# Kernel optimization log

Hardware: AMD Instinct MI355X
Metric: run time of the kernel (lower is better)

## Reference

```python
import jax, jax.numpy as jnp
import numpy as np

B, S, D, H = 4, 2048, 1024, 16
HD = D // H  # head dim = 64

def setup_inputs() -> dict:
    key = jax.random.key(0)
    ks = jax.random.split(key, 11)
    s = 1.0 / np.sqrt(D)
    return {
        "q": jax.random.normal(ks[0], (B, S, D), jnp.float32),
        "k": jax.random.normal(ks[1], (B, S, D), jnp.float32),
        "v": jax.random.normal(ks[2], (B, S, D), jnp.float32),
        "Wq": jax.random.normal(ks[3], (D, D), jnp.float32) * s,
        "bq": jnp.zeros((D,), jnp.float32),
        "Wk": jax.random.normal(ks[4], (D, D), jnp.float32) * s,
        "bk": jnp.zeros((D,), jnp.float32),
        "Wv": jax.random.normal(ks[5], (D, D), jnp.float32) * s,
        "bv": jnp.zeros((D,), jnp.float32),
        "Wo": jax.random.normal(ks[6], (D, D), jnp.float32) * s,
        "bo": jnp.zeros((D,), jnp.float32),
    }

def reference(q, k, v, Wq, bq, Wk, bk, Wv, bv, Wo, bo):
    b, n, _ = q.shape
    # QKV projections, split heads -> [b, s, h, hd]
    qh = (q @ Wq + bq).reshape(b, n, H, HD)
    kh = (k @ Wk + bk).reshape(b, k.shape[1], H, HD)
    vh = (v @ Wv + bv).reshape(b, v.shape[1], H, HD)
    scale = 1.0 / np.sqrt(HD)
    scores = jnp.einsum('blhe,bshe->bhls', qh, kh)  # [b,h,l,s]
    attn = jax.nn.softmax(scale * scores, axis=-1)  # dropout is identity in eval
    out = jnp.einsum('bhls,bshd->blhd', attn, vh)   # [b,l,h,hd]
    out = out.reshape(b, n, H * HD)
    return out @ Wo + bo
```

## Files before the change

kernel.cpp:

```cpp
#include <hip/hip_runtime.h>
#include <cstdint>

#define DEV __device__ __forceinline__

typedef __attribute__((ext_vector_type(8))) __bf16 bf16x8;
typedef __attribute__((ext_vector_type(8))) _Float16 f16x8;
typedef __attribute__((ext_vector_type(2))) __fp16 fp16x2;
typedef __attribute__((ext_vector_type(2))) unsigned u32x2;
typedef __attribute__((ext_vector_type(4))) float f32x4;

DEV unsigned short f2b(float f) {
  unsigned u = __builtin_bit_cast(unsigned, f);
  u += 0x7fffu + ((u >> 16) & 1u);
  return (unsigned short)(u >> 16);
}

DEV unsigned pkhf(float a, float b) {
  fp16x2 h = __builtin_amdgcn_cvt_pkrtz(a, b);
  return __builtin_bit_cast(unsigned, h);
}

DEV float exp2_fast(float x) {
#if __has_builtin(__builtin_amdgcn_exp2f)
  return __builtin_amdgcn_exp2f(x);
#else
  return __expf(x * 0.6931471805599453f);
#endif
}

DEV void gload_lds16(const unsigned short* g, unsigned short* l) {
  __builtin_amdgcn_global_load_lds(
      (const __attribute__((address_space(1))) void*)g,
      (__attribute__((address_space(3))) void*)l, 16, 0, 0);
}

__global__ __launch_bounds__(256) void cvt3_kernel(const float* __restrict__ q,
                                                   const float* __restrict__ k,
                                                   const float* __restrict__ v,
                                                   unsigned short* __restrict__ dst) {
  int z = blockIdx.y;
  const float* src = (z == 0) ? q : (z == 1) ? k : v;
  unsigned short* d = dst + (size_t)z * 8192 * 1024;
  int i = blockIdx.x * 256 + threadIdx.x;
  const float4* s4 = (const float4*)src;
  float4 a = s4[2 * i], b = s4[2 * i + 1];
  uint4 o;
  o.x = (unsigned)f2b(a.x) | ((unsigned)f2b(a.y) << 16);
  o.y = (unsigned)f2b(a.z) | ((unsigned)f2b(a.w) << 16);
  o.z = (unsigned)f2b(b.x) | ((unsigned)f2b(b.y) << 16);
  o.w = (unsigned)f2b(b.z) | ((unsigned)f2b(b.w) << 16);
  ((uint4*)d)[i] = o;
}

__global__ __launch_bounds__(256) void wtr4_kernel(const float* __restrict__ W0,
                                                   const float* __restrict__ W1,
                                                   const float* __restrict__ W2,
                                                   const float* __restrict__ W3,
                                                   unsigned short* __restrict__ WtBase) {
  int z = blockIdx.z;
  const float* W = (z == 0) ? W0 : (z == 1) ? W1 : (z == 2) ? W2 : W3;
  unsigned short* Wt = WtBase + (size_t)z * 1024 * 1024;
  __shared__ float t[64][65];
  int n0 = blockIdx.x * 64, k0 = blockIdx.y * 64;
  int tx = threadIdx.x & 63, ty = threadIdx.x >> 6;
  for (int i = ty; i < 64; i += 4)
    t[i][tx] = W[(size_t)(k0 + i) * 1024 + n0 + tx];
  __syncthreads();
  for (int i = ty; i < 64; i += 4)
    Wt[(size_t)(n0 + i) * 1024 + k0 + tx] = f2b(t[tx][i]);
}

struct GemmAcc {
  f32x4 acc[4][4];
};

DEV void gemm_core(const unsigned short* __restrict__ A,
                   const unsigned short* __restrict__ Bt,
                   unsigned short* Al, unsigned short* Bl,
                   int m0, int n0, int K, GemmAcc& R) {
  int tid = threadIdx.x, wv = tid >> 6, ln = tid & 63;
  int wr = wv >> 1, wc = wv & 1;
  for (int i = 0; i < 4; i++)
    for (int j = 0; j < 4; j++) R.acc[i][j] = (f32x4)0.f;
  int lr = ln >> 3, lc = (ln & 7) * 8;
  for (int kt = 0; kt < K; kt += 64) {
    __syncthreads();
    for (int o = 0; o < 4; ++o) {
      int op = wv * 4 + o;
      int row = op * 8 + lr;
      gload_lds16(A + (size_t)(m0 + row) * K + kt + lc, &Al[op * 512]);
    }
    for (int o = 0; o < 4; ++o) {
      int op = wv * 4 + o;
      int row = op * 8 + lr;
      gload_lds16(Bt + (size_t)(n0 + row) * K + kt + lc, &Bl[op * 512]);
    }
    __syncthreads();
    for (int kk = 0; kk < 2; ++kk) {
      bf16x8 af[4], bfr[4];
      int ko = kk * 32 + (ln >> 4) * 8;
      for (int i = 0; i < 4; ++i)
        af[i] = *(const bf16x8*)&Al[(wr * 64 + i * 16 + (ln & 15)) * 64 + ko];
      for (int j = 0; j < 4; ++j)
        bfr[j] = *(const bf16x8*)&Bl[(wc * 64 + j * 16 + (ln & 15)) * 64 + ko];
      for (int i = 0; i < 4; ++i)
        for (int j = 0; j < 4; ++j)
          R.acc[i][j] = __builtin_amdgcn_mfma_f32_16x16x32_bf16(af[i], bfr[j], R.acc[i][j], 0, 0, 0);
    }
  }
}

__global__ __launch_bounds__(256) void gemm_qkv(const unsigned short* __restrict__ Xbase,
                                                const unsigned short* __restrict__ Wbase,
                                                const float* __restrict__ bq,
                                                const float* __restrict__ bk,
                                                const float* __restrict__ bv,
                                                unsigned short* __restrict__ Obase,
                                                float qscale) {
  __shared__ unsigned short Al[128 * 64];
  __shared__ unsigned short Bl[128 * 64];
  int z = blockIdx.z;
  const size_t NX = (size_t)8192 * 1024, NW = (size_t)1024 * 1024;
  const unsigned short* A = Xbase + (size_t)z * NX;
  const unsigned short* Bt = Wbase + (size_t)z * NW;
  const float* bias = (z == 0) ? bq : (z == 1) ? bk : bv;
  unsigned short* outp = Obase + (size_t)z * NX;
  int m0 = blockIdx.y * 128, n0 = blockIdx.x * 128;
  GemmAcc R;
  gemm_core(A, Bt, Al, Bl, m0, n0, 1024, R);
  int ln = threadIdx.x & 63, wv = threadIdx.x >> 6;
  int wr = wv >> 1, wc = wv & 1;
  int g = ln >> 4, c = ln & 15;
  int mb = m0 + wr * 64;
  int b_ = mb >> 11, sb = mb & 2047;
  if (z < 2) {
    float oscale = (z == 0) ? qscale : 1.0f;
    for (int j = 0; j < 4; ++j) {
      int gn = n0 + wc * 64 + j * 16 + c;
      float bs = bias[gn];
      int h_ = gn >> 6, hd = gn & 63;
      unsigned short* base = outp + (((size_t)(b_ * 16 + h_) * 2048 + sb + g * 4) << 6) + hd;
      for (int i = 0; i < 4; ++i)
        for (int r = 0; r < 4; ++r)
          base[i * 1024 + r * 64] = f2b((R.acc[i][j][r] + bs) * oscale);
    }
  } else {
    int st = sb >> 6;
    for (int j = 0; j < 4; ++j) {
      int gn = n0 + wc * 64 + j * 16 + c;
      float bs = bias[gn];
      int h_ = gn >> 6, hd = gn & 63;
      unsigned short* vrow = outp + (((size_t)((b_ * 16 + h_) * 32 + st) * 64 + hd) << 6);
      for (int r = 0; r < 4; ++r) {
        u32x2 w;
        w.x = pkhf(R.acc[0][j][r] + bs, R.acc[1][j][r] + bs);
        w.y = pkhf(R.acc[2][j][r] + bs, R.acc[3][j][r] + bs);
        *(u32x2*)&vrow[(g * 4 + r) * 4] = w;
      }
    }
  }
}

__global__ __launch_bounds__(256) void gemm_out(const unsigned short* __restrict__ A,
                                                const unsigned short* __restrict__ Bt,
                                                const float* __restrict__ bias,
                                                float* __restrict__ outp) {
  __shared__ unsigned short Al[128 * 64];
  __shared__ unsigned short Bl[128 * 64];
  int m0 = blockIdx.y * 128, n0 = blockIdx.x * 128;
  GemmAcc R;
  gemm_core(A, Bt, Al, Bl, m0, n0, 1024, R);
  int ln = threadIdx.x & 63, wv = threadIdx.x >> 6;
  int wr = wv >> 1, wc = wv & 1;
  int g = ln >> 4, c = ln & 15;
  for (int j = 0; j < 4; ++j) {
    int gn = n0 + wc * 64 + j * 16 + c;
    float bs = bias[gn];
    float* base = outp + (size_t)(m0 + wr * 64 + g * 4) * 1024 + gn;
    for (int i = 0; i < 4; ++i)
      for (int r = 0; r < 4; ++r)
        base[(i * 16 + r) * 1024] = R.acc[i][j][r] + bs;
  }
}

__global__ __launch_bounds__(256) void attn_kernel(const unsigned short* __restrict__ Qh,
                                                   const unsigned short* __restrict__ Kh,
                                                   const unsigned short* __restrict__ VtG,
                                                   unsigned short* __restrict__ AttnOut) {
  __shared__ unsigned short Kl[2 * 64 * 64];
  __shared__ unsigned short Vl[2 * 64 * 64];
  __shared__ unsigned short Pl[4 * 32 * 72];
  int tid = threadIdx.x, wv = tid >> 6, ln = tid & 63;
  int qt = blockIdx.x, bh = blockIdx.y;
  const unsigned short* Qb = Qh + (size_t)bh * 2048 * 64;
  const unsigned short* Kb = Kh + (size_t)bh * 2048 * 64;
  const unsigned short* Vb = VtG + (size_t)bh * 2048 * 64;
  int q0 = qt * 128 + wv * 32;
  int g = ln >> 4, c = ln & 15;
  int lr = ln >> 3, lb = ln & 7;
  int swz = (lb ^ lr) * 8;
  bf16x8 aq[2][2];
  for (int mi = 0; mi < 2; ++mi)
    for (int kk = 0; kk < 2; ++kk)
      aq[mi][kk] = *(const bf16x8*)(Qb + (size_t)(q0 + mi * 16 + c) * 64 + kk * 32 + g * 8);
  f32x4 o[2][4], ladd[2];
  for (int mi = 0; mi < 2; ++mi) {
    ladd[mi] = (f32x4)0.f;
    for (int j = 0; j < 4; ++j) o[mi][j] = (f32x4)0.f;
  }
  const f32x4 z4 = {0.f, 0.f, 0.f, 0.f};
  f16x8 ones;
  for (int i = 0; i < 8; ++i) ones[i] = (_Float16)1.0f;
  unsigned short* pw = &Pl[wv * 32 * 72];
  int boff[2][4];
  for (int kk = 0; kk < 2; ++kk)
    for (int j = 0; j < 4; ++j) boff[kk][j] = (j * 16 + c) * 64 + (((kk * 4 + g) ^ (c & 7)) * 8);
  int aoff[2][2];
  for (int mi = 0; mi < 2; ++mi)
    for (int kk = 0; kk < 2; ++kk) aoff[mi][kk] = (mi * 16 + c) * 72 + kk * 32 + g * 8;
  int poff[2][4];
  for (int mi = 0; mi < 2; ++mi)
    for (int r = 0; r < 4; ++r) poff[mi][r] = (mi * 16 + g * 4 + r) * 72 + c * 4;
  int rb0 = wv * 16, rb1 = wv * 16 + 8;
  gload_lds16(Kb + (size_t)(rb0 + lr) * 64 + swz, &Kl[rb0 * 64]);
  gload_lds16(Kb + (size_t)(rb1 + lr) * 64 + swz, &Kl[rb1 * 64]);
  gload_lds16(Vb + (size_t)(rb0 + lr) * 64 + swz, &Vl[rb0 * 64]);
  gload_lds16(Vb + (size_t)(rb1 + lr) * 64 + swz, &Vl[rb1 * 64]);
  const unsigned short* kg0 = Kb + 4096 + (size_t)(rb0 + lr) * 64 + swz;
  const unsigned short* kg1 = Kb + 4096 + (size_t)(rb1 + lr) * 64 + swz;
  const unsigned short* vg0 = Vb + 4096 + (size_t)(rb0 + lr) * 64 + swz;
  const unsigned short* vg1 = Vb + 4096 + (size_t)(rb1 + lr) * 64 + swz;
  for (int t = 0; t < 32; ++t) {
    __syncthreads();
    int cur = (t & 1) * 4096;
    if (t + 1 < 32) {
      int nxt = cur ^ 4096;
      gload_lds16(kg0, &Kl[nxt + rb0 * 64]);
      gload_lds16(kg1, &Kl[nxt + rb1 * 64]);
      gload_lds16(vg0, &Vl[nxt + rb0 * 64]);
      gload_lds16(vg1, &Vl[nxt + rb1 * 64]);
      kg0 += 4096; kg1 += 4096; vg0 += 4096; vg1 += 4096;
    }
    f32x4 s[2][4];
    {
      bf16x8 bk[4];
      for (int j = 0; j < 4; ++j) bk[j] = *(const bf16x8*)&Kl[cur + boff[0][j]];
      for (int mi = 0; mi < 2; ++mi)
        for (int j = 0; j < 4; ++j)
          s[mi][j] = __builtin_amdgcn_mfma_f32_16x16x32_bf16(aq[mi][0], bk[j], z4, 0, 0, 0);
      for (int j = 0; j < 4; ++j) bk[j] = *(const bf16x8*)&Kl[cur + boff[1][j]];
      for (int mi = 0; mi < 2; ++mi)
        for (int j = 0; j < 4; ++j)
          s[mi][j] = __builtin_amdgcn_mfma_f32_16x16x32_bf16(aq[mi][1], bk[j], s[mi][j], 0, 0, 0);
    }
    for (int mi = 0; mi < 2; ++mi)
      for (int r = 0; r < 4; ++r) {
        u32x2 w;
        w.x = pkhf(exp2_fast(s[mi][0][r]), exp2_fast(s[mi][1][r]));
        w.y = pkhf(exp2_fast(s[mi][2][r]), exp2_fast(s[mi][3][r]));
        *(u32x2*)&pw[poff[mi][r]] = w;
      }
    __threadfence_block();
    for (int kk = 0; kk < 2; ++kk) {
      f16x8 ap[2], bv[4];
      for (int mi = 0; mi < 2; ++mi) ap[mi] = *(const f16x8*)&pw[aoff[mi][kk]];
      for (int j = 0; j < 4; ++j) bv[j] = *(const f16x8*)&Vl[cur + boff[kk][j]];
      for (int mi = 0; mi < 2; ++mi)
        ladd[mi] = __builtin_amdgcn_mfma_f32_16x16x32_f16(ap[mi], ones, ladd[mi], 0, 0, 0);
      for (int mi = 0; mi < 2; ++mi)
        for (int j = 0; j < 4; ++j)
          o[mi][j] = __builtin_amdgcn_mfma_f32_16x16x32_f16(ap[mi], bv[j], o[mi][j], 0, 0, 0);
    }
  }
  int b_ = bh >> 4, h_ = bh & 15;
  for (int mi = 0; mi < 2; ++mi) {
    float linv[4];
    for (int r = 0; r < 4; ++r) linv[r] = 1.f / ladd[mi][r];
    for (int j = 0; j < 4; ++j)
      for (int r = 0; r < 4; ++r) {
        int row = q0 + mi * 16 + g * 4 + r;
        int col = h_ * 64 + j * 16 + c;
        float val = o[mi][j][r] * linv[r];
        AttnOut[((size_t)b_ * 2048 + row) * 1024 + col] = f2b(val);
      }
  }
}

extern "C" void kernel_launch(void* const* d_in, const int* in_sizes, int n_in,
                              void* d_out, int out_size, void* d_ws, size_t ws_size,
                              hipStream_t stream) {
  const float* q  = (const float*)d_in[0];
  const float* k  = (const float*)d_in[1];
  const float* v  = (const float*)d_in[2];
  const float* Wq = (const float*)d_in[3];
  const float* bq = (const float*)d_in[4];
  const float* Wk = (const float*)d_in[5];
  const float* bk = (const float*)d_in[6];
  const float* Wv = (const float*)d_in[7];
  const float* bv = (const float*)d_in[8];
  const float* Wo = (const float*)d_in[9];
  const float* bo = (const float*)d_in[10];
  float* out = (float*)d_out;

  unsigned short* ws = (unsigned short*)d_ws;
  const size_t NX = (size_t)8192 * 1024;
  const size_t NW = (size_t)1024 * 1024;
  unsigned short* X   = ws;
  unsigned short* Wt  = X + 3 * NX;
  unsigned short* QKV = Wt + 4 * NW;
  unsigned short* Ao  = X;

  const float qscale = 0.125f * 1.4426950408889634f;

  cvt3_kernel<<<dim3(4096, 3), 256, 0, stream>>>(q, k, v, X);
  wtr4_kernel<<<dim3(16, 16, 4), 256, 0, stream>>>(Wq, Wk, Wv, Wo, Wt);
  gemm_qkv<<<dim3(8, 64, 3), 256, 0, stream>>>(X, Wt, bq, bk, bv, QKV, qscale);
  attn_kernel<<<dim3(16, 64), 256, 0, stream>>>(QKV, QKV + NX, QKV + 2 * NX, Ao);
  gemm_out<<<dim3(8, 64), 256, 0, stream>>>(Ao, Wt + 3 * NW, bo, out);
}
```

Baseline: 389.2 us.

## Use 512-thread attention blocks with single-buffered K/V and a shuffle-reduced row sum

```diff
diff --git a/kernel.cpp b/kernel.cpp
--- a/kernel.cpp
+++ b/kernel.cpp
@@ -183,19 +183,19 @@
   }
 }
 
-__global__ __launch_bounds__(256) void attn_kernel(const unsigned short* __restrict__ Qh,
-                                                   const unsigned short* __restrict__ Kh,
-                                                   const unsigned short* __restrict__ VtG,
-                                                   unsigned short* __restrict__ AttnOut) {
-  __shared__ unsigned short Kl[2 * 64 * 64];
-  __shared__ unsigned short Vl[2 * 64 * 64];
-  __shared__ unsigned short Pl[4 * 32 * 72];
+__global__ __launch_bounds__(512, 6) void attn_kernel(const unsigned short* __restrict__ Qh,
+                                                      const unsigned short* __restrict__ Kh,
+                                                      const unsigned short* __restrict__ VtG,
+                                                      unsigned short* __restrict__ AttnOut) {
+  __shared__ unsigned short Kl[64 * 64];
+  __shared__ unsigned short Vl[64 * 64];
+  __shared__ unsigned short Pl[8 * 32 * 72];
   int tid = threadIdx.x, wv = tid >> 6, ln = tid & 63;
   int qt = blockIdx.x, bh = blockIdx.y;
   const unsigned short* Qb = Qh + (size_t)bh * 2048 * 64;
   const unsigned short* Kb = Kh + (size_t)bh * 2048 * 64;
   const unsigned short* Vb = VtG + (size_t)bh * 2048 * 64;
-  int q0 = qt * 128 + wv * 32;
+  int q0 = qt * 256 + wv * 32;
   int g = ln >> 4, c = ln & 15;
   int lr = ln >> 3, lb = ln & 7;
   int swz = (lb ^ lr) * 8;
@@ -203,14 +203,12 @@
   for (int mi = 0; mi < 2; ++mi)
     for (int kk = 0; kk < 2; ++kk)
       aq[mi][kk] = *(const bf16x8*)(Qb + (size_t)(q0 + mi * 16 + c) * 64 + kk * 32 + g * 8);
-  f32x4 o[2][4], ladd[2];
+  f32x4 o[2][4], lrun[2];
   for (int mi = 0; mi < 2; ++mi) {
-    ladd[mi] = (f32x4)0.f;
+    lrun[mi] = (f32x4)0.f;
     for (int j = 0; j < 4; ++j) o[mi][j] = (f32x4)0.f;
   }
   const f32x4 z4 = {0.f, 0.f, 0.f, 0.f};
-  f16x8 ones;
-  for (int i = 0; i < 8; ++i) ones[i] = (_Float16)1.0f;
   unsigned short* pw = &Pl[wv * 32 * 72];
   int boff[2][4];
   for (int kk = 0; kk < 2; ++kk)
@@ -221,52 +219,47 @@
   int poff[2][4];
   for (int mi = 0; mi < 2; ++mi)
     for (int r = 0; r < 4; ++r) poff[mi][r] = (mi * 16 + g * 4 + r) * 72 + c * 4;
-  int rb0 = wv * 16, rb1 = wv * 16 + 8;
-  gload_lds16(Kb + (size_t)(rb0 + lr) * 64 + swz, &Kl[rb0 * 64]);
-  gload_lds16(Kb + (size_t)(rb1 + lr) * 64 + swz, &Kl[rb1 * 64]);
-  gload_lds16(Vb + (size_t)(rb0 + lr) * 64 + swz, &Vl[rb0 * 64]);
-  gload_lds16(Vb + (size_t)(rb1 + lr) * 64 + swz, &Vl[rb1 * 64]);
-  const unsigned short* kg0 = Kb + 4096 + (size_t)(rb0 + lr) * 64 + swz;
-  const unsigned short* kg1 = Kb + 4096 + (size_t)(rb1 + lr) * 64 + swz;
-  const unsigned short* vg0 = Vb + 4096 + (size_t)(rb0 + lr) * 64 + swz;
-  const unsigned short* vg1 = Vb + 4096 + (size_t)(rb1 + lr) * 64 + swz;
+  int rb = wv * 8;
+  const unsigned short* kg = Kb + (size_t)(rb + lr) * 64 + swz;
+  const unsigned short* vg = Vb + (size_t)(rb + lr) * 64 + swz;
+  unsigned short* kl = &Kl[rb * 64];
+  unsigned short* vl = &Vl[rb * 64];
   for (int t = 0; t < 32; ++t) {
     __syncthreads();
-    int cur = (t & 1) * 4096;
-    if (t + 1 < 32) {
-      int nxt = cur ^ 4096;
-      gload_lds16(kg0, &Kl[nxt + rb0 * 64]);
-      gload_lds16(kg1, &Kl[nxt + rb1 * 64]);
-      gload_lds16(vg0, &Vl[nxt + rb0 * 64]);
-      gload_lds16(vg1, &Vl[nxt + rb1 * 64]);
-      kg0 += 4096; kg1 += 4096; vg0 += 4096; vg1 += 4096;
-    }
+    gload_lds16(kg, kl);
+    gload_lds16(vg, vl);
+    kg += 4096;
+    vg += 4096;
+    __syncthreads();
     f32x4 s[2][4];
     {
       bf16x8 bk[4];
-      for (int j = 0; j < 4; ++j) bk[j] = *(const bf16x8*)&Kl[cur + boff[0][j]];
+      for (int j = 0; j < 4; ++j) bk[j] = *(const bf16x8*)&Kl[boff[0][j]];
       for (int mi = 0; mi < 2; ++mi)
         for (int j = 0; j < 4; ++j)
           s[mi][j] = __builtin_amdgcn_mfma_f32_16x16x32_bf16(aq[mi][0], bk[j], z4, 0, 0, 0);
-      for (int j = 0; j < 4; ++j) bk[j] = *(const bf16x8*)&Kl[cur + boff[1][j]];
+      for (int j = 0; j < 4; ++j) bk[j] = *(const bf16x8*)&Kl[boff[1][j]];
       for (int mi = 0; mi < 2; ++mi)
         for (int j = 0; j < 4; ++j)
           s[mi][j] = __builtin_amdgcn_mfma_f32_16x16x32_bf16(aq[mi][1], bk[j], s[mi][j], 0, 0, 0);
     }
     for (int mi = 0; mi < 2; ++mi)
       for (int r = 0; r < 4; ++r) {
+        float p0 = exp2_fast(s[mi][0][r]);
+        float p1 = exp2_fast(s[mi][1][r]);
+        float p2 = exp2_fast(s[mi][2][r]);
+        float p3 = exp2_fast(s[mi][3][r]);
+        lrun[mi][r] += (p0 + p1) + (p2 + p3);
         u32x2 w;
-        w.x = pkhf(exp2_fast(s[mi][0][r]), exp2_fast(s[mi][1][r]));
-        w.y = pkhf(exp2_fast(s[mi][2][r]), exp2_fast(s[mi][3][r]));
+        w.x = pkhf(p0, p1);
+        w.y = pkhf(p2, p3);
         *(u32x2*)&pw[poff[mi][r]] = w;
       }
     __threadfence_block();
     for (int kk = 0; kk < 2; ++kk) {
       f16x8 ap[2], bv[4];
       for (int mi = 0; mi < 2; ++mi) ap[mi] = *(const f16x8*)&pw[aoff[mi][kk]];
-      for (int j = 0; j < 4; ++j) bv[j] = *(const f16x8*)&Vl[cur + boff[kk][j]];
-      for (int mi = 0; mi < 2; ++mi)
-        ladd[mi] = __builtin_amdgcn_mfma_f32_16x16x32_f16(ap[mi], ones, ladd[mi], 0, 0, 0);
+      for (int j = 0; j < 4; ++j) bv[j] = *(const f16x8*)&Vl[boff[kk][j]];
       for (int mi = 0; mi < 2; ++mi)
         for (int j = 0; j < 4; ++j)
           o[mi][j] = __builtin_amdgcn_mfma_f32_16x16x32_f16(ap[mi], bv[j], o[mi][j], 0, 0, 0);
@@ -275,7 +268,11 @@
   int b_ = bh >> 4, h_ = bh & 15;
   for (int mi = 0; mi < 2; ++mi) {
     float linv[4];
-    for (int r = 0; r < 4; ++r) linv[r] = 1.f / ladd[mi][r];
+    for (int r = 0; r < 4; ++r) {
+      float l = lrun[mi][r];
+      for (int d = 1; d < 16; d <<= 1) l += __shfl_xor(l, d);
+      linv[r] = 1.f / l;
+    }
     for (int j = 0; j < 4; ++j)
       for (int r = 0; r < 4; ++r) {
         int row = q0 + mi * 16 + g * 4 + r;
@@ -315,6 +312,6 @@
   cvt3_kernel<<<dim3(4096, 3), 256, 0, stream>>>(q, k, v, X);
   wtr4_kernel<<<dim3(16, 16, 4), 256, 0, stream>>>(Wq, Wk, Wv, Wo, Wt);
   gemm_qkv<<<dim3(8, 64, 3), 256, 0, stream>>>(X, Wt, bq, bk, bv, QKV, qscale);
-  attn_kernel<<<dim3(16, 64), 256, 0, stream>>>(QKV, QKV + NX, QKV + 2 * NX, Ao);
+  attn_kernel<<<dim3(8, 64), 512, 0, stream>>>(QKV, QKV + NX, QKV + 2 * NX, Ao);
   gemm_out<<<dim3(8, 64), 256, 0, stream>>>(Ao, Wt + 3 * NW, bo, out);
 }
```

Result: slower. 739.4 us (+90.0%).
